# Performance work log

Hardware: AMD Instinct MI355X
Metric: run time of the kernel (lower is better)

Reference implementation:

```python
import jax, jax.numpy as jnp
import numpy as np

B, LQ, LKV = 8, 512, 512
D, H, DH, FF = 1024, 16, 64, 4096
CH, CHID = 16, 32  # AttentionBiasMLP channels
EPS_LOG = 1e-6
EPS_LN = 1e-6


def _ln(x, g, b):
    mu = jnp.mean(x, axis=-1, keepdims=True)
    var = jnp.var(x, axis=-1, keepdims=True)
    return (x - mu) * jax.lax.rsqrt(var + EPS_LN) * g + b


def setup_inputs() -> dict:
    key = jax.random.key(0)
    ks = jax.random.split(key, 24)
    s = 0.02
    inp = {
        "q": jax.random.normal(ks[0], (B, LQ, D), jnp.float32),
        "kv": jax.random.normal(ks[1], (B, LKV, D), jnp.float32),
        "attn_map": jax.random.uniform(ks[2], (B, CH, LQ + 1, LKV + 1), jnp.float32),
        # attention projections (torch Linear: y = x @ W.T + b)
        "Wq": jax.random.normal(ks[3], (D, D)) * s, "bq": jnp.zeros((D,)),
        "Wk": jax.random.normal(ks[4], (D, D)) * s, "bk": jnp.zeros((D,)),
        "Wv": jax.random.normal(ks[5], (D, D)) * s, "bv": jnp.zeros((D,)),
        "Wm": jax.random.normal(ks[6], (D, D)) * s, "bm": jnp.zeros((D,)),
        # AttentionBiasMLP 1x1 convs: weight [out_ch, in_ch]
        "Wc1": jax.random.normal(ks[7], (CHID, CH)) * s, "bc1": jnp.zeros((CHID,)),
        "Wc2": jax.random.normal(ks[8], (CH, CHID)) * s, "bc2": jnp.zeros((CH,)),
        # FFN: Linear(D,FF) -> ReLU -> Linear(FF,D)
        "Wf1": jax.random.normal(ks[9], (FF, D)) * s, "bf1": jnp.zeros((FF,)),
        "Wf2": jax.random.normal(ks[10], (D, FF)) * s, "bf2": jnp.zeros((D,)),
        # LayerNorms
        "g1": jnp.ones((D,)), "b1": jnp.zeros((D,)),
        "g2": jnp.ones((D,)), "b2": jnp.zeros((D,)),
    }
    return inp


def _forward(q, kv, attn_map, Wq, bq, Wk, bk, Wv, bv, Wm, bm,
             Wc1, bc1, Wc2, bc2, Wf1, bf1, Wf2, bf2, g1, b1, g2, b2):
    # attention bias: log of cropped attn_map through 1x1-conv MLP with exact GELU
    log_map = jnp.log(attn_map[:, :, 1:, 1:] + EPS_LOG)               # [B,CH,LQ,LKV]
    h = jnp.einsum('bcqk,oc->boqk', log_map, Wc1) + bc1[None, :, None, None]
    h = jax.nn.gelu(h, approximate=False)
    attn_bias = jnp.einsum('bcqk,oc->boqk', h, Wc2) + bc2[None, :, None, None]

    # MHAtt: project, split heads
    qh = (q @ Wq.T + bq).reshape(B, LQ, H, DH).transpose(0, 2, 1, 3)   # [B,H,LQ,DH]
    kh = (kv @ Wk.T + bk).reshape(B, LKV, H, DH).transpose(0, 2, 1, 3)
    vh = (kv @ Wv.T + bv).reshape(B, LKV, H, DH).transpose(0, 2, 1, 3)

    scores = jnp.einsum('bhqd,bhkd->bhqk', qh, kh) / np.sqrt(DH).astype(np.float32)
    scores = scores + attn_bias
    att = jax.nn.softmax(scores, axis=-1)
    ctx = jnp.einsum('bhqk,bhkd->bhqd', att, vh)                       # [B,H,LQ,DH]
    ctx = ctx.transpose(0, 2, 1, 3).reshape(B, LQ, D)
    atted = ctx @ Wm.T + bm

    x = _ln(q + atted, g1, b1)
    ffn = jax.nn.relu(x @ Wf1.T + bf1) @ Wf2.T + bf2
    x = _ln(x + ffn, g2, b2)
    return x


def reference(q, kv, attn_map, Wq, bq, Wk, bk, Wv, bv, Wm, bm,
              Wc1, bc1, Wc2, bc2, Wf1, bf1, Wf2, bf2, g1, b1, g2, b2):
    return _forward(q, kv, attn_map, Wq, bq, Wk, bk, Wv, bv, Wm, bm,
                    Wc1, bc1, Wc2, bc2, Wf1, bf1, Wf2, bf2, g1, b1, g2, b2)
```

## Files before the change

### kernel.cpp

```cpp
#include <hip/hip_runtime.h>
#include <hip/hip_bf16.h>

typedef __bf16 bf16_t;
typedef __bf16 bf16x4_t __attribute__((ext_vector_type(4)));
typedef __bf16 bf16x8_t __attribute__((ext_vector_type(8)));
typedef float  f32x4_t  __attribute__((ext_vector_type(4)));

#define B_   8
#define LQ_  512
#define LKV_ 512
#define D_   1024
#define H_   16
#define DH_  64
#define FF_  4096

__device__ __forceinline__ f32x4_t mfma16(bf16x8_t a, bf16x8_t b, f32x4_t c) {
    return __builtin_amdgcn_mfma_f32_16x16x32_bf16(a, b, c, 0, 0, 0);
}

__device__ __forceinline__ void gload_lds16(const bf16_t* g, bf16_t* l) {
    __builtin_amdgcn_global_load_lds(
        (const __attribute__((address_space(1))) void*)g,
        (__attribute__((address_space(3))) void*)l, 16, 0, 0);
}

__device__ __forceinline__ int xcd_swz(int pid, int nwg) {
    return (pid & 7) * (nwg >> 3) + (pid >> 3);
}

__device__ __forceinline__ float gelu_fast(float h) {
    const float e = exp2f(h * -2.45546696f);
    return h * __builtin_amdgcn_rcpf(1.f + e);
}

__global__ __launch_bounds__(256)
void cvt_all_kernel(const float* __restrict__ q,  const float* __restrict__ kv,
                    const float* __restrict__ Wq, const float* __restrict__ Wk,
                    const float* __restrict__ Wv, const float* __restrict__ Wm,
                    const float* __restrict__ Wf1,const float* __restrict__ Wf2,
                    bf16_t* __restrict__ dq, bf16_t* __restrict__ dW,
                    bf16_t* __restrict__ dF) {
    const int i = blockIdx.x * 256 + threadIdx.x;
    const float* s; bf16_t* d; int j;
    if (i < 1048576)      { s = q;   d = dq;           j = i; }
    else if (i < 2097152) { s = kv;  d = dq + 4194304; j = i - 1048576; }
    else if (i < 2359296) { s = Wq;  d = dW;           j = i - 2097152; }
    else if (i < 2621440) { s = Wk;  d = dW + 1048576; j = i - 2359296; }
    else if (i < 2883584) { s = Wv;  d = dW + 2097152; j = i - 2621440; }
    else if (i < 3145728) { s = Wm;  d = dW + 3145728; j = i - 2883584; }
    else if (i < 4194304) { s = Wf1; d = dF;           j = i - 3145728; }
    else                  { s = Wf2; d = dF + 4194304; j = i - 4194304; }
    const float4 v = ((const float4*)s)[j];
    bf16x4_t o;
    o[0] = (bf16_t)v.x; o[1] = (bf16_t)v.y; o[2] = (bf16_t)v.z; o[3] = (bf16_t)v.w;
    ((bf16x4_t*)d)[j] = o;
}

__global__ __launch_bounds__(256)
void pack3_kernel(const float* __restrict__ a, const float* __restrict__ b,
                  const float* __restrict__ c, float* __restrict__ o) {
    const int i = blockIdx.x * 256 + threadIdx.x;
    o[i] = a[i]; o[1024 + i] = b[i]; o[2048 + i] = c[i];
}

__global__ __launch_bounds__(256)
void bias_mlp_mfma(const float* __restrict__ amap,
                   const float* __restrict__ Wc1, const float* __restrict__ bc1,
                   const float* __restrict__ Wc2, const float* __restrict__ bc2,
                   bf16_t* __restrict__ biasb) {
    __shared__ __align__(16) char lds[4][8192];
    const int t = threadIdx.x, lane = t & 63, w = t >> 6;
    const int l15 = lane & 15, lg = lane >> 4;
    char* Xs = lds[w];
    char* Hs = lds[w] + 3072;

    bf16x8_t b1f[2], b2f;
    f32x4_t bc1v[2];
#pragma unroll
    for (int ot = 0; ot < 2; ot++) {
        bf16x8_t v;
#pragma unroll
        for (int i = 0; i < 8; i++) {
            const int kk = (lg * 8 + i) & 15;
            const float wv = Wc1[(ot * 16 + l15) * 16 + kk] * 0.69314718055994531f;
            v[i] = (lg < 2) ? (bf16_t)wv : (bf16_t)0.f;
        }
        b1f[ot] = v;
        const float bb = bc1[ot * 16 + l15];
        bc1v[ot] = f32x4_t{bb, bb, bb, bb};
    }
    {
        bf16x8_t v;
#pragma unroll
        for (int i = 0; i < 8; i++) v[i] = (bf16_t)Wc2[l15 * 32 + lg * 8 + i];
        b2f = v;
    }
    const float bc2s = bc2[l15];
    const f32x4_t cinit2 = f32x4_t{bc2s, bc2s, bc2s, bc2s};

    const int posb = (blockIdx.x * 4 + w) * 64;
    const int b  = posb >> 18;
    const int q  = (posb >> 9) & 511;
    const int k0 = posb & 511;

    const float* src = amap + (size_t)(b * 16) * 263169 + (size_t)(q + 1) * 513 + (k0 + 1 + lane);
    bf16_t xr[16];
#pragma unroll
    for (int c = 0; c < 16; c++) {
        const float v = src[(size_t)c * 263169];
        xr[c] = (bf16_t)__log2f(v + 1e-6f);
    }
    *(bf16x8_t*)(Xs + lane * 48)      = *(bf16x8_t*)&xr[0];
    *(bf16x8_t*)(Xs + lane * 48 + 16) = *(bf16x8_t*)&xr[8];

    const int lgm16 = (lg & 1) * 16;
    f32x4_t h1[4][2];
#pragma unroll
    for (int p = 0; p < 4; p++) {
        const bf16x8_t a1 = *(const bf16x8_t*)(Xs + (p * 16 + l15) * 48 + lgm16);
#pragma unroll
        for (int ot = 0; ot < 2; ot++)
            h1[p][ot] = mfma16(a1, b1f[ot], bc1v[ot]);
    }

#pragma unroll
    for (int p = 0; p < 4; p++)
#pragma unroll
        for (int ot = 0; ot < 2; ot++)
#pragma unroll
            for (int r = 0; r < 4; r++) {
                const float g = gelu_fast(h1[p][ot][r]);
                *(bf16_t*)(Hs + (p * 16 + lg * 4 + r) * 80 + (ot * 16 + l15) * 2) = (bf16_t)g;
            }

    const size_t obase = ((size_t)(b * 16 + l15) * 512 + q) * 512 + k0;
#pragma unroll
    for (int p = 0; p < 4; p++) {
        const bf16x8_t a2 = *(const bf16x8_t*)(Hs + (p * 16 + l15) * 80 + lg * 16);
        const f32x4_t o2 = mfma16(a2, b2f, cinit2);
        bf16x4_t ov;
#pragma unroll
        for (int r = 0; r < 4; r++) ov[r] = (bf16_t)o2[r];
        *(bf16x4_t*)&biasb[obase + p * 16 + lg * 4] = ov;
    }
}

template <int EPI, bool SPLIT>
__global__ __launch_bounds__(256)
void gemm_bt(const bf16_t* __restrict__ A, const bf16_t* __restrict__ A2,
             const bf16_t* __restrict__ Bw,
             const float* __restrict__ bias,
             bf16_t* __restrict__ Cb, int M, int N, int Klen, int lda) {
    __shared__ __align__(16) bf16_t As[3][128 * 32];
    __shared__ __align__(16) bf16_t Bs[3][128 * 32];
    const int t = threadIdx.x, lane = t & 63, w = t >> 6;
    const int wr = w >> 1, wc = w & 1;
    const int ntn = N >> 7;
    const int nwg = (M >> 7) * ntn;
    const int wg  = xcd_swz((int)blockIdx.x, nwg);
    const int gsz = 8 * ntn;
    const int gid = wg / gsz;
    const int rem = wg - gid * gsz;
    const int tm  = gid * 8 + (rem & 7);
    const int tn  = rem >> 3;
    const int l15 = lane & 15, lg = lane >> 4;
    const int ks = SPLIT ? blockIdx.y : 0;
    const int koff = SPLIT ? ks * Klen : 0;
    if (EPI == 3 && tn >= 8) A = A2;

    const int r0 = t >> 2,          k0 = t & 3;
    const int r1 = (t + 256) >> 2,  k1 = t & 3;
    const int b0 = (w * 64) * 8;
    const int b1 = (256 + w * 64) * 8;
    const bf16_t* Abase0 = A  + (size_t)(tm * 128 + r0) * lda + koff + k0 * 8;
    const bf16_t* Abase1 = A  + (size_t)(tm * 128 + r1) * lda + koff + k1 * 8;
    const bf16_t* Bbase0 = Bw + (size_t)(tn * 128 + r0) * lda + koff + k0 * 8;
    const bf16_t* Bbase1 = Bw + (size_t)(tn * 128 + r1) * lda + koff + k1 * 8;

    f32x4_t acc[4][4];
#pragma unroll
    for (int i = 0; i < 4; i++)
#pragma unroll
        for (int j = 0; j < 4; j++) acc[i][j] = f32x4_t{0.f, 0.f, 0.f, 0.f};

    const int nk = Klen >> 5;

#define STAGE(KT, S)                                    \
    do {                                                \
        const int _ko = (KT) * 32;                      \
        gload_lds16(Abase0 + _ko, &As[(S)][b0]);        \
        gload_lds16(Abase1 + _ko, &As[(S)][b1]);        \
        gload_lds16(Bbase0 + _ko, &Bs[(S)][b0]);        \
        gload_lds16(Bbase1 + _ko, &Bs[(S)][b1]);        \
    } while (0)

    STAGE(0, 0);
    STAGE(1, 1);

    int cur = 0;
    for (int kt = 0; kt < nk; ++kt) {
        if (kt + 1 < nk) { asm volatile("s_waitcnt vmcnt(4)" ::: "memory"); }
        else             { asm volatile("s_waitcnt vmcnt(0)" ::: "memory"); }
        __syncthreads();
        if (kt + 2 < nk) {
            const int s2 = cur >= 1 ? cur - 1 : cur + 2;
            STAGE(kt + 2, s2);
        }

        const bf16_t* Ac = As[cur];
        const bf16_t* Bc = Bs[cur];
        bf16x8_t af[4], bfv[4];
#pragma unroll
        for (int mt = 0; mt < 4; mt++)
            af[mt] = *(const bf16x8_t*)&Ac[(wr * 64 + mt * 16 + l15) * 32 + lg * 8];
#pragma unroll
        for (int nt = 0; nt < 4; nt++)
            bfv[nt] = *(const bf16x8_t*)&Bc[(wc * 64 + nt * 16 + l15) * 32 + lg * 8];
#pragma unroll
        for (int mt = 0; mt < 4; mt++)
#pragma unroll
            for (int nt = 0; nt < 4; nt++)
                acc[mt][nt] = mfma16(af[mt], bfv[nt], acc[mt][nt]);

        cur = cur < 2 ? cur + 1 : 0;
    }
#undef STAGE

#pragma unroll
    for (int nt = 0; nt < 4; nt++) {
        const int col = tn * 128 + wc * 64 + nt * 16 + l15;
        float bv = bias[col];
        if (SPLIT && ks != 0) bv = 0.f;
#pragma unroll
        for (int mt = 0; mt < 4; mt++) {
#pragma unroll
            for (int r = 0; r < 4; r++) {
                const int row = tm * 128 + wr * 64 + mt * 16 + lg * 4 + r;
                float v = acc[mt][nt][r] + bv;
                if (EPI == 2) v = fmaxf(v, 0.f);
                if (EPI == 3 && tn < 8) v *= 0.125f;
                if (SPLIT)
                    Cb[(size_t)ks * M * N + (size_t)row * N + col] = (bf16_t)v;
                else if (EPI == 3)
                    Cb[(size_t)(col >> 10) * 4194304 + (size_t)row * 1024 + (col & 1023)] = (bf16_t)v;
                else Cb[(size_t)row * N + col] = (bf16_t)v;
            }
        }
    }
}

__global__ __launch_bounds__(256)
void attn_kernel(const bf16_t* __restrict__ Qp, const bf16_t* __restrict__ Kp,
                 const bf16_t* __restrict__ Vp, const bf16_t* __restrict__ biasb,
                 bf16_t* __restrict__ ctx) {
    __shared__ __align__(16) bf16_t Qs[64 * 64];
    __shared__ __align__(16) bf16_t Ks[64 * 64];
    __shared__ __align__(16) bf16_t Vts[64 * 64];
    __shared__ __align__(16) bf16_t Ps[64 * 64];
    __shared__ __align__(16) bf16_t Bbs[64 * 64];

    const int bid = xcd_swz((int)blockIdx.x, 1024);
    const int qt = bid & 7, h = (bid >> 3) & 15, b = bid >> 7;
    const int t = threadIdx.x, lane = t & 63, w = t >> 6;
    const int l15 = lane & 15, lg = lane >> 4;

#pragma unroll
    for (int i = 0; i < 2; i++) {
        const int c = t + i * 256;
        const int row = c >> 3, cg = c & 7;
        const uint4 v = *(const uint4*)&Qp[(((size_t)(b * LQ_ + qt * 64 + row)) * H_ + h) * DH_ + cg * 8];
        *(uint4*)((char*)Qs + row * 128 + ((cg ^ (row & 7)) << 4)) = v;
    }
    __syncthreads();

    bf16x8_t aq[2];
    {
        const int rowq = w * 16 + l15;
#pragma unroll
        for (int kc = 0; kc < 2; kc++)
            aq[kc] = *(const bf16x8_t*)((const char*)Qs + rowq * 128 + (((kc * 4 + lg) ^ (rowq & 7)) << 4));
    }

    f32x4_t oacc[4];
#pragma unroll
    for (int i = 0; i < 4; i++) oacc[i] = f32x4_t{0.f, 0.f, 0.f, 0.f};
    float mrow[4] = {-1e30f, -1e30f, -1e30f, -1e30f};
    float lrow[4] = {0.f, 0.f, 0.f, 0.f};

    const bf16_t* bias_tile = biasb + ((size_t)(b * H_ + h) * LQ_ + qt * 64) * LKV_;

    for (int kt = 0; kt < 8; ++kt) {
        __syncthreads();
#pragma unroll
        for (int i = 0; i < 2; i++) {
            const int c = t + i * 256;
            const int row = c >> 3, cg = c & 7;
            const uint4 v = *(const uint4*)&Kp[(((size_t)(b * LKV_ + kt * 64 + row)) * H_ + h) * DH_ + cg * 8];
            *(uint4*)((char*)Ks + row * 128 + ((cg ^ (row & 7)) << 4)) = v;
        }
#pragma unroll
        for (int i = 0; i < 2; i++) {
            const int c = t + i * 256;
            const int row = c >> 3, cg = c & 7;
            const uint4 bv4 = *(const uint4*)&bias_tile[(size_t)row * LKV_ + kt * 64 + cg * 8];
            *(uint4*)&Bbs[row * 64 + cg * 8] = bv4;
        }
#pragma unroll
        for (int i = 0; i < 2; i++) {
            const int c = t + i * 256;
            const int k = c >> 3, dg = c & 7;
            const bf16x8_t vv = *(const bf16x8_t*)&Vp[(((size_t)(b * LKV_ + kt * 64 + k)) * H_ + h) * DH_ + dg * 8];
#pragma unroll
            for (int j = 0; j < 8; j++) {
                const int d = dg * 8 + j;
                *(bf16_t*)((char*)Vts + d * 128 + ((((k * 2) >> 4) ^ (d & 7)) << 4) + ((k * 2) & 15)) = vv[j];
            }
        }
        __syncthreads();

        f32x4_t sacc[4];
#pragma unroll
        for (int i = 0; i < 4; i++) sacc[i] = f32x4_t{0.f, 0.f, 0.f, 0.f};
#pragma unroll
        for (int nt = 0; nt < 4; nt++) {
            const int rowk = nt * 16 + l15;
#pragma unroll
            for (int kc = 0; kc < 2; kc++) {
                const bf16x8_t bk = *(const bf16x8_t*)((const char*)Ks + rowk * 128 + (((kc * 4 + lg) ^ (rowk & 7)) << 4));
                sacc[nt] = mfma16(aq[kc], bk, sacc[nt]);
            }
        }

        float esc[4];
#pragma unroll
        for (int r = 0; r < 4; r++) {
            const int qr = w * 16 + lg * 4 + r;
            float mx = -1e30f;
#pragma unroll
            for (int nt = 0; nt < 4; nt++) {
                const float bvv = (float)Bbs[qr * 64 + nt * 16 + l15];
                const float v = sacc[nt][r] + bvv;
                sacc[nt][r] = v;
                mx = fmaxf(mx, v);
            }
#pragma unroll
            for (int msk = 8; msk >= 1; msk >>= 1) mx = fmaxf(mx, __shfl_xor(mx, msk));
            const float mnew = fmaxf(mrow[r], mx);
            esc[r] = __expf(mrow[r] - mnew);
            mrow[r] = mnew;
            float rs = 0.f;
#pragma unroll
            for (int nt = 0; nt < 4; nt++) {
                const float p = __expf(sacc[nt][r] - mnew);
                sacc[nt][r] = p;
                rs += p;
            }
#pragma unroll
            for (int msk = 8; msk >= 1; msk >>= 1) rs += __shfl_xor(rs, msk);
            lrow[r] = lrow[r] * esc[r] + rs;
        }

#pragma unroll
        for (int r = 0; r < 4; r++) {
            const int prow = w * 16 + lg * 4 + r;
#pragma unroll
            for (int nt = 0; nt < 4; nt++) {
                const int pc2 = (nt * 16 + l15) * 2;
                *(bf16_t*)((char*)Ps + prow * 128 + (((pc2 >> 4) ^ (prow & 7)) << 4) + (pc2 & 15)) =
                    (bf16_t)sacc[nt][r];
            }
        }
        asm volatile("s_waitcnt lgkmcnt(0)" ::: "memory");
        __builtin_amdgcn_sched_barrier(0);

#pragma unroll
        for (int dt = 0; dt < 4; dt++)
#pragma unroll
            for (int r = 0; r < 4; r++) oacc[dt][r] *= esc[r];

        bf16x8_t pa[2];
        {
            const int rowp = w * 16 + l15;
#pragma unroll
            for (int kc = 0; kc < 2; kc++)
                pa[kc] = *(const bf16x8_t*)((const char*)Ps + rowp * 128 + (((kc * 4 + lg) ^ (rowp & 7)) << 4));
        }
#pragma unroll
        for (int dt = 0; dt < 4; dt++) {
            const int rowv = dt * 16 + l15;
#pragma unroll
            for (int kc = 0; kc < 2; kc++) {
                const bf16x8_t bv = *(const bf16x8_t*)((const char*)Vts + rowv * 128 + (((kc * 4 + lg) ^ (rowv & 7)) << 4));
                oacc[dt] = mfma16(pa[kc], bv, oacc[dt]);
            }
        }
    }

    float inv[4];
#pragma unroll
    for (int r = 0; r < 4; r++) inv[r] = __builtin_amdgcn_rcpf(lrow[r]);
#pragma unroll
    for (int dt = 0; dt < 4; dt++) {
#pragma unroll
        for (int r = 0; r < 4; r++) {
            const float v = oacc[dt][r] * inv[r];
            const int q = qt * 64 + w * 16 + lg * 4 + r;
            const int d = dt * 16 + l15;
            ctx[(((size_t)(b * LQ_ + q)) * H_ + h) * DH_ + d] = (bf16_t)v;
        }
    }
}

__global__ __launch_bounds__(256)
void add_ln3_kernel(const float* __restrict__ X, const bf16_t* __restrict__ Y0,
                    const bf16_t* __restrict__ Y1,
                    const float* __restrict__ g, const float* __restrict__ be,
                    float* __restrict__ of, bf16_t* __restrict__ ob) {
    const int row = blockIdx.x, t = threadIdx.x;
    const float4 xv = ((const float4*)(X + (size_t)row * 1024))[t];
    const bf16x4_t y0 = ((const bf16x4_t*)(Y0 + (size_t)row * 1024))[t];
    const bf16x4_t y1 = ((const bf16x4_t*)(Y1 + (size_t)row * 1024))[t];
    float v[4] = {xv.x + (float)y0[0] + (float)y1[0], xv.y + (float)y0[1] + (float)y1[1],
                  xv.z + (float)y0[2] + (float)y1[2], xv.w + (float)y0[3] + (float)y1[3]};
    float s = v[0] + v[1] + v[2] + v[3];
    float s2 = v[0] * v[0] + v[1] * v[1] + v[2] * v[2] + v[3] * v[3];
#pragma unroll
    for (int m = 32; m >= 1; m >>= 1) { s += __shfl_xor(s, m); s2 += __shfl_xor(s2, m); }
    __shared__ float red[8];
    const int w = t >> 6, lane = t & 63;
    if (lane == 0) { red[w] = s; red[4 + w] = s2; }
    __syncthreads();
    s = red[0] + red[1] + red[2] + red[3];
    s2 = red[4] + red[5] + red[6] + red[7];
    const float mu = s * (1.f / 1024.f);
    const float var = s2 * (1.f / 1024.f) - mu * mu;
    const float rstd = rsqrtf(var + 1e-6f);
    const float4 gv = ((const float4*)g)[t];
    const float4 bv = ((const float4*)be)[t];
    float o[4];
    o[0] = (v[0] - mu) * rstd * gv.x + bv.x;
    o[1] = (v[1] - mu) * rstd * gv.y + bv.y;
    o[2] = (v[2] - mu) * rstd * gv.z + bv.z;
    o[3] = (v[3] - mu) * rstd * gv.w + bv.w;
    ((float4*)(of + (size_t)row * 1024))[t] = make_float4(o[0], o[1], o[2], o[3]);
    if (ob) {
        bf16x4_t qo;
        qo[0] = (bf16_t)o[0]; qo[1] = (bf16_t)o[1]; qo[2] = (bf16_t)o[2]; qo[3] = (bf16_t)o[3];
        ((bf16x4_t*)(ob + (size_t)row * 1024))[t] = qo;
    }
}

extern "C" void kernel_launch(void* const* d_in, const int* in_sizes, int n_in,
                              void* d_out, int out_size, void* d_ws, size_t ws_size,
                              hipStream_t stream) {
    (void)in_sizes; (void)n_in; (void)out_size; (void)ws_size;
    const float* q    = (const float*)d_in[0];
    const float* kv   = (const float*)d_in[1];
    const float* amap = (const float*)d_in[2];
    const float* Wq = (const float*)d_in[3];  const float* bQ = (const float*)d_in[4];
    const float* Wk = (const float*)d_in[5];  const float* bK = (const float*)d_in[6];
    const float* Wv = (const float*)d_in[7];  const float* bV = (const float*)d_in[8];
    const float* Wm = (const float*)d_in[9];  const float* bM = (const float*)d_in[10];
    const float* Wc1 = (const float*)d_in[11]; const float* bc1 = (const float*)d_in[12];
    const float* Wc2 = (const float*)d_in[13]; const float* bc2 = (const float*)d_in[14];
    const float* Wf1 = (const float*)d_in[15]; const float* bf1 = (const float*)d_in[16];
    const float* Wf2 = (const float*)d_in[17]; const float* bf2 = (const float*)d_in[18];
    const float* g1 = (const float*)d_in[19]; const float* b1 = (const float*)d_in[20];
    const float* g2 = (const float*)d_in[21]; const float* b2 = (const float*)d_in[22];

    char* w = (char*)d_ws;
    bf16_t* biasb = (bf16_t*)(w);
    bf16_t* p0    = (bf16_t*)(w);
    bf16_t* p1    = (bf16_t*)(w + 8388608);
    bf16_t* hb    = (bf16_t*)(w);
    bf16_t* f0    = (bf16_t*)(w + 33554432);
    bf16_t* f1    = (bf16_t*)(w + 41943040);
    bf16_t* qb   = (bf16_t*)(w + 67108864);
    bf16_t* kvb  = (bf16_t*)(w + 75497472);
    bf16_t* Qp   = (bf16_t*)(w + 83886080);
    bf16_t* Kp   = (bf16_t*)(w + 92274688);
    bf16_t* Vp   = (bf16_t*)(w + 100663296);
    bf16_t* Wqkvb = (bf16_t*)(w + 109051904);
    bf16_t* Wmb  = (bf16_t*)(w + 115343360);
    bf16_t* Wf1b = (bf16_t*)(w + 117440512);
    bf16_t* Wf2b = (bf16_t*)(w + 125829120);
    float*  bqkv = (float*)(w + 134217728);
    bf16_t* ctx = qb;
    float*  xf  = (float*)Qp;
    bf16_t* xb  = Vp;

    dim3 blk(256);
    cvt_all_kernel<<<20480, blk, 0, stream>>>(q, kv, Wq, Wk, Wv, Wm, Wf1, Wf2,
                                              qb, Wqkvb, Wf1b);
    pack3_kernel<<<4, blk, 0, stream>>>(bQ, bK, bV, bqkv);

    bias_mlp_mfma<<<8192, blk, 0, stream>>>(amap, Wc1, bc1, Wc2, bc2, biasb);

    gemm_bt<3, false><<<768, blk, 0, stream>>>(qb, kvb, Wqkvb, bqkv, Qp,
                                               4096, 3072, 1024, 1024);

    attn_kernel<<<1024, blk, 0, stream>>>(Qp, Kp, Vp, biasb, ctx);

    gemm_bt<0, true><<<dim3(256, 2), blk, 0, stream>>>(ctx, nullptr, Wmb, bM, p0,
                                                       4096, 1024, 512, 1024);
    add_ln3_kernel<<<4096, blk, 0, stream>>>(q, p0, p1, g1, b1, xf, xb);

    gemm_bt<2, false><<<1024, blk, 0, stream>>>(xb, nullptr, Wf1b, bf1, hb,
                                                4096, 4096, 1024, 1024);
    gemm_bt<0, true><<<dim3(256, 2), blk, 0, stream>>>(hb, nullptr, Wf2b, bf2, f0,
                                                       4096, 1024, 2048, 4096);
    add_ln3_kernel<<<4096, blk, 0, stream>>>(xf, f0, f1, g2, b2, (float*)d_out, nullptr);
}
```

Before: 329.9 us.

## Add 256x256-tile 8-wave GEMM for QKV and FFN1 projections

New measurement: 369.0 us. +11.8%, slower.

```diff
diff --git a/kernel.cpp b/kernel.cpp
--- a/kernel.cpp
+++ b/kernel.cpp
@@ -166,7 +166,6 @@
     const int l15 = lane & 15, lg = lane >> 4;
     const int ks = SPLIT ? blockIdx.y : 0;
     const int koff = SPLIT ? ks * Klen : 0;
-    if (EPI == 3 && tn >= 8) A = A2;
 
     const int r0 = t >> 2,          k0 = t & 3;
     const int r1 = (t + 256) >> 2,  k1 = t & 3;
@@ -185,7 +184,7 @@
 
     const int nk = Klen >> 5;
 
-#define STAGE(KT, S)                                    \
+#define STAGE128(KT, S)                                 \
     do {                                                \
         const int _ko = (KT) * 32;                      \
         gload_lds16(Abase0 + _ko, &As[(S)][b0]);        \
@@ -194,8 +193,8 @@
         gload_lds16(Bbase1 + _ko, &Bs[(S)][b1]);        \
     } while (0)
 
-    STAGE(0, 0);
-    STAGE(1, 1);
+    STAGE128(0, 0);
+    STAGE128(1, 1);
 
     int cur = 0;
     for (int kt = 0; kt < nk; ++kt) {
@@ -204,7 +203,7 @@
         __syncthreads();
         if (kt + 2 < nk) {
             const int s2 = cur >= 1 ? cur - 1 : cur + 2;
-            STAGE(kt + 2, s2);
+            STAGE128(kt + 2, s2);
         }
 
         const bf16_t* Ac = As[cur];
@@ -224,7 +223,7 @@
 
         cur = cur < 2 ? cur + 1 : 0;
     }
-#undef STAGE
+#undef STAGE128
 
 #pragma unroll
     for (int nt = 0; nt < 4; nt++) {
@@ -238,12 +237,123 @@
                 const int row = tm * 128 + wr * 64 + mt * 16 + lg * 4 + r;
                 float v = acc[mt][nt][r] + bv;
                 if (EPI == 2) v = fmaxf(v, 0.f);
-                if (EPI == 3 && tn < 8) v *= 0.125f;
                 if (SPLIT)
                     Cb[(size_t)ks * M * N + (size_t)row * N + col] = (bf16_t)v;
-                else if (EPI == 3)
+                else Cb[(size_t)row * N + col] = (bf16_t)v;
+            }
+        }
+    }
+}
+
+template <int EPI>
+__global__ __launch_bounds__(512, 1)
+void gemm8p(const bf16_t* __restrict__ A, const bf16_t* __restrict__ A2,
+            const bf16_t* __restrict__ Bw, const float* __restrict__ bias,
+            bf16_t* __restrict__ Cb, int M, int N, int Klen, int lda) {
+    __shared__ __align__(16) bf16_t As[2][256 * 64];
+    __shared__ __align__(16) bf16_t Bs[2][256 * 64];
+    const int t = threadIdx.x, lane = t & 63, w = t >> 6;
+    const int wr = w >> 2, wc = w & 3;
+    const int l15 = lane & 15, lg = lane >> 4;
+    const int ntn = N >> 8;
+    const int nwg = (M >> 8) * ntn;
+    const int wg  = xcd_swz((int)blockIdx.x, nwg);
+    const int gsz = 8 * ntn;
+    const int gid = wg / gsz;
+    const int rem = wg - gid * gsz;
+    const int tm  = gid * 8 + (rem & 7);
+    const int tn  = rem >> 3;
+    if (EPI == 3 && tn >= 4) A = A2;
+
+    const int srow = w * 8 + (lane >> 3);
+    const int scol = (lane & 7) * 8;
+    const bf16_t* Ag = A  + (size_t)(tm * 256 + srow) * lda + scol;
+    const bf16_t* Bg = Bw + (size_t)(tn * 256 + srow) * lda + scol;
+    const int ldsb = w * 512;
+
+#define STAGE256(KT, S)                                                      \
+    do {                                                                     \
+        const size_t _ko = (size_t)(KT) * 64;                                \
+        _Pragma("unroll")                                                    \
+        for (int _i = 0; _i < 4; _i++) {                                     \
+            gload_lds16(Ag + (size_t)(_i * 64) * lda + _ko,                  \
+                        &As[(S)][_i * 4096 + ldsb]);                         \
+            gload_lds16(Bg + (size_t)(_i * 64) * lda + _ko,                  \
+                        &Bs[(S)][_i * 4096 + ldsb]);                         \
+        }                                                                    \
+    } while (0)
+
+    f32x4_t acc[8][4];
+#pragma unroll
+    for (int i = 0; i < 8; i++)
+#pragma unroll
+        for (int j = 0; j < 4; j++) acc[i][j] = f32x4_t{0.f, 0.f, 0.f, 0.f};
+
+    const int nk = Klen >> 6;
+
+    STAGE256(0, 0);
+    STAGE256(1, 1);
+
+    for (int kt = 0; kt < nk; ++kt) {
+        const int s = kt & 1;
+        if (kt + 1 < nk) { asm volatile("s_waitcnt vmcnt(8)" ::: "memory"); }
+        else             { asm volatile("s_waitcnt vmcnt(0)" ::: "memory"); }
+        __builtin_amdgcn_s_barrier();
+        __builtin_amdgcn_sched_barrier(0);
+
+#pragma unroll
+        for (int q = 0; q < 4; q++) {
+            const int mh = q >> 1, nh = q & 1;
+            bf16x8_t af[4][2], bfv[2][2];
+#pragma unroll
+            for (int mi = 0; mi < 4; mi++) {
+                const int row = wr * 128 + (mh * 4 + mi) * 16 + l15;
+#pragma unroll
+                for (int kk = 0; kk < 2; kk++)
+                    af[mi][kk] = *(const bf16x8_t*)&As[s][row * 64 + kk * 32 + lg * 8];
+            }
+#pragma unroll
+            for (int ni = 0; ni < 2; ni++) {
+                const int row = wc * 64 + (nh * 2 + ni) * 16 + l15;
+#pragma unroll
+                for (int kk = 0; kk < 2; kk++)
+                    bfv[ni][kk] = *(const bf16x8_t*)&Bs[s][row * 64 + kk * 32 + lg * 8];
+            }
+            __builtin_amdgcn_s_setprio(1);
+#pragma unroll
+            for (int mi = 0; mi < 4; mi++)
+#pragma unroll
+                for (int ni = 0; ni < 2; ni++)
+#pragma unroll
+                    for (int kk = 0; kk < 2; kk++)
+                        acc[mh * 4 + mi][nh * 2 + ni] =
+                            mfma16(af[mi][kk], bfv[ni][kk], acc[mh * 4 + mi][nh * 2 + ni]);
+            __builtin_amdgcn_s_setprio(0);
+        }
+
+        __builtin_amdgcn_sched_barrier(0);
+        __builtin_amdgcn_s_barrier();
+        __builtin_amdgcn_sched_barrier(0);
+        if (kt + 2 < nk) STAGE256(kt + 2, s);
+    }
+#undef STAGE256
+
+#pragma unroll
+    for (int n = 0; n < 4; n++) {
+        const int col = tn * 256 + wc * 64 + n * 16 + l15;
+        const float bv = bias[col];
+#pragma unroll
+        for (int m = 0; m < 8; m++) {
+#pragma unroll
+            for (int r = 0; r < 4; r++) {
+                const int row = tm * 256 + wr * 128 + m * 16 + lg * 4 + r;
+                float v = acc[m][n][r] + bv;
+                if (EPI == 2) v = fmaxf(v, 0.f);
+                if (EPI == 3 && tn < 4) v *= 0.125f;
+                if (EPI == 3)
                     Cb[(size_t)(col >> 10) * 4194304 + (size_t)row * 1024 + (col & 1023)] = (bf16_t)v;
-                else Cb[(size_t)row * N + col] = (bf16_t)v;
+                else
+                    Cb[(size_t)row * N + col] = (bf16_t)v;
             }
         }
     }
@@ -496,8 +606,8 @@
 
     bias_mlp_mfma<<<8192, blk, 0, stream>>>(amap, Wc1, bc1, Wc2, bc2, biasb);
 
-    gemm_bt<3, false><<<768, blk, 0, stream>>>(qb, kvb, Wqkvb, bqkv, Qp,
-                                               4096, 3072, 1024, 1024);
+    gemm8p<3><<<192, dim3(512), 0, stream>>>(qb, kvb, Wqkvb, bqkv, Qp,
+                                             4096, 3072, 1024, 1024);
 
     attn_kernel<<<1024, blk, 0, stream>>>(Qp, Kp, Vp, biasb, ctx);
 
@@ -505,8 +615,8 @@
                                                        4096, 1024, 512, 1024);
     add_ln3_kernel<<<4096, blk, 0, stream>>>(q, p0, p1, g1, b1, xf, xb);
 
-    gemm_bt<2, false><<<1024, blk, 0, stream>>>(xb, nullptr, Wf1b, bf1, hb,
-                                                4096, 4096, 1024, 1024);
+    gemm8p<2><<<256, dim3(512), 0, stream>>>(xb, nullptr, Wf1b, bf1, hb,
+                                             4096, 4096, 1024, 1024);
     gemm_bt<0, true><<<dim3(256, 2), blk, 0, stream>>>(hb, nullptr, Wf2b, bf2, f0,
                                                        4096, 1024, 2048, 4096);
     add_ln3_kernel<<<4096, blk, 0, stream>>>(xf, f0, f1, g2, b2, (float*)d_out, nullptr);
```
